# Kernel optimization log

Hardware: AMD Instinct MI355X
Metric: run time of the kernel (lower is better)

## Reference

```python
import jax, jax.numpy as jnp
import numpy as np

N, C, K, G, E = 65536, 256, 128, 32, 2097152
LN_EPS = 1e-5


def setup_inputs() -> dict:
    key = jax.random.key(0)
    ks = jax.random.split(key, 16)
    inp = {
        "x": jax.random.normal(ks[0], (N, C), jnp.float32),
        "evals_batch": jax.random.uniform(ks[1], (G * K,), jnp.float32),
        "evecs": jax.random.normal(ks[2], (N, K), jnp.float32),
        "mass": jax.random.uniform(ks[3], (N,), jnp.float32),
        "row": jax.random.randint(ks[4], (E,), 0, N),
        "col": jax.random.randint(ks[5], (E,), 0, N),
        "vals": jax.random.normal(ks[6], (E,), jnp.float32),
        # learned parameters (torch Linear convention: weight is [out, in])
        "t_params": jnp.full((C,), 0.5, jnp.float32),
        "grad_W": jax.random.normal(ks[7], (C, C), jnp.float32) / np.sqrt(C),
        "grad_b": jnp.zeros((C,), jnp.float32),
        "W1": jax.random.normal(ks[8], (C, 2 * C), jnp.float32) / np.sqrt(2 * C),
        "b1": jnp.zeros((C,), jnp.float32),
        "W2": jax.random.normal(ks[9], (C, C), jnp.float32) / np.sqrt(C),
        "b2": jnp.zeros((C,), jnp.float32),
        "ln_g": jnp.ones((C,), jnp.float32),
        "ln_b": jnp.zeros((C,), jnp.float32),
    }
    return inp


def reference(x, evals_batch, evecs, mass, row, col, vals,
              t_params, grad_W, grad_b, W1, b1, W2, b2, ln_g, ln_b):
    # batch is contiguous with G equal-size graphs of n nodes each
    n = N // G
    t = jnp.abs(t_params)                                   # [C]
    xg = x.reshape(G, n, C)
    eg = evecs.reshape(G, n, K)
    mg = mass.reshape(G, n)
    ev = evals_batch.reshape(G, K)
    # spectral diffusion, batched over graphs
    x_spec = jnp.einsum('gnk,gnc->gkc', eg, xg * mg[..., None])      # [G,K,C]
    decay = jnp.exp(-t[None, None, :] * jnp.clip(ev, 0.0)[..., None])  # [G,K,C]
    diff_out = jnp.einsum('gnk,gkc->gnc', eg, x_spec * decay).reshape(N, C)
    # sparse gradient operator: grad_feat = grad_X_sparse @ x  (COO)
    grad_feat = jax.ops.segment_sum(vals[:, None] * x[col], row, num_segments=N)
    grad_feat = grad_feat @ grad_W.T + grad_b
    # MLP (dropout is identity at eval)
    fused = jnp.concatenate([diff_out, grad_feat], axis=-1)           # [N,2C]
    h = jax.nn.relu(fused @ W1.T + b1)
    fused = h @ W2.T + b2
    # residual + LayerNorm
    y = x + fused
    mu = jnp.mean(y, axis=-1, keepdims=True)
    var = jnp.var(y, axis=-1, keepdims=True)
    return (y - mu) * jax.lax.rsqrt(var + LN_EPS) * ln_g + ln_b
```

## Files before the change

### kernel.cpp

```cpp
#include <hip/hip_runtime.h>

typedef unsigned short u16;
typedef unsigned long long u64;
using short8 = __attribute__((ext_vector_type(8))) short;
using f32x4  = __attribute__((ext_vector_type(4))) float;

constexpr int N_  = 65536;
constexpr int C_  = 256;
constexpr int K_  = 128;
constexpr int G_  = 32;
constexpr int NG_ = 2048;
constexpr int E_  = 2097152;
constexpr int NBIN_ = 2048;
constexpr int CAPB_ = 1280;
constexpr int NCHK_ = 256;

__device__ __forceinline__ u16 f2bf(float f) {
  unsigned u = __float_as_uint(f);
  unsigned r = u + 0x7FFF + ((u >> 16) & 1);
  return (u16)(r >> 16);
}
__device__ __forceinline__ float bf2f(u16 h) { return __uint_as_float((unsigned)h << 16); }

__device__ __forceinline__ void gload_lds16(const void* g, void* l) {
  __builtin_amdgcn_global_load_lds((const __attribute__((address_space(1))) void*)g,
                                   (__attribute__((address_space(3))) void*)l, 16, 0, 0);
}

constexpr int PA_HIST = NCHK_;
constexpr int PA_CVX  = 4096;
constexpr int PA_CVE  = 2048;
constexpr int PA_W1   = 512;
constexpr int PA_W2   = 256;
constexpr int PA_T256 = 16;
constexpr int PA_BC   = 16;
constexpr int PA_TOTAL = PA_HIST + PA_CVX + PA_CVE + PA_W1 + PA_W2 + PA_T256 + PA_BC;

__global__ __launch_bounds__(256) void k_phaseA(
    const int* __restrict__ row, int* __restrict__ bh,
    const float* __restrict__ x, const float* __restrict__ mass,
    u16* __restrict__ xbf, u16* __restrict__ xmT,
    const float* __restrict__ evecs, u16* __restrict__ Ebf, u16* __restrict__ EbfT,
    const float* __restrict__ W1, u16* __restrict__ W1bf,
    const float* __restrict__ W2, u16* __restrict__ W2bf,
    const float* __restrict__ gW, u16* __restrict__ gWT,
    const float* __restrict__ gb, const float* __restrict__ b1, float* __restrict__ bc) {
  __shared__ __align__(16) char smem[64 * 65 * 4 + 256];
  float (*tile)[65] = (float(*)[65])smem;
  float* msm = (float*)(smem + 64 * 65 * 4);
  int id = blockIdx.x, tid = threadIdx.x;

  if (id < PA_HIST) {
    int* hist = (int*)smem;
    #pragma unroll
    for (int j = 0; j < 8; ++j) hist[tid + j * 256] = 0;
    __syncthreads();
    int e0 = id * 8192 + tid;
    #pragma unroll 4
    for (int i = 0; i < 32; ++i)
      atomicAdd(&hist[row[e0 + i * 256] >> 5], 1);
    __syncthreads();
    #pragma unroll
    for (int j = 0; j < 8; ++j) {
      int bin = tid + j * 256;
      bh[(size_t)bin * NCHK_ + id] = hist[bin];
    }
    return;
  }
  id -= PA_HIST;
  if (id < PA_CVX) {
    int r0 = (id >> 2) * 64, c0 = (id & 3) * 64;
    int tr = tid >> 4, tc4 = (tid & 15) * 4;
    #pragma unroll
    for (int p = 0; p < 4; ++p) {
      int r = p * 16 + tr;
      float4 v = *(const float4*)&x[(size_t)(r0 + r) * C_ + c0 + tc4];
      tile[r][tc4 + 0] = v.x; tile[r][tc4 + 1] = v.y; tile[r][tc4 + 2] = v.z; tile[r][tc4 + 3] = v.w;
      ushort4 o = {f2bf(v.x), f2bf(v.y), f2bf(v.z), f2bf(v.w)};
      *(ushort4*)&xbf[(size_t)(r0 + r) * C_ + c0 + tc4] = o;
    }
    if (tid < 64) msm[tid] = mass[r0 + tid];
    __syncthreads();
    int g = r0 >> 11, n0 = r0 & (NG_ - 1);
    #pragma unroll
    for (int p = 0; p < 4; ++p) {
      int cl = p * 16 + tr;
      ushort4 o;
      o.x = f2bf(tile[tc4 + 0][cl] * msm[tc4 + 0]);
      o.y = f2bf(tile[tc4 + 1][cl] * msm[tc4 + 1]);
      o.z = f2bf(tile[tc4 + 2][cl] * msm[tc4 + 2]);
      o.w = f2bf(tile[tc4 + 3][cl] * msm[tc4 + 3]);
      *(ushort4*)&xmT[((size_t)g * C_ + c0 + cl) * NG_ + n0 + tc4] = o;
    }
    return;
  }
  id -= PA_CVX;
  if (id < PA_CVE) {
    int r0 = (id >> 1) * 64, c0 = (id & 1) * 64;
    int tr = tid >> 4, tc4 = (tid & 15) * 4;
    #pragma unroll
    for (int p = 0; p < 4; ++p) {
      int r = p * 16 + tr;
      float4 v = *(const float4*)&evecs[(size_t)(r0 + r) * K_ + c0 + tc4];
      tile[r][tc4 + 0] = v.x; tile[r][tc4 + 1] = v.y; tile[r][tc4 + 2] = v.z; tile[r][tc4 + 3] = v.w;
      ushort4 o = {f2bf(v.x), f2bf(v.y), f2bf(v.z), f2bf(v.w)};
      *(ushort4*)&Ebf[(size_t)(r0 + r) * K_ + c0 + tc4] = o;
    }
    __syncthreads();
    int g = r0 >> 11, n0 = r0 & (NG_ - 1);
    #pragma unroll
    for (int p = 0; p < 4; ++p) {
      int cl = p * 16 + tr;
      ushort4 o = {f2bf(tile[tc4 + 0][cl]), f2bf(tile[tc4 + 1][cl]),
                   f2bf(tile[tc4 + 2][cl]), f2bf(tile[tc4 + 3][cl])};
      *(ushort4*)&EbfT[((size_t)g * K_ + c0 + cl) * NG_ + n0 + tc4] = o;
    }
    return;
  }
  id -= PA_CVE;
  if (id < PA_W1) { int i = id * 256 + tid; W1bf[i] = f2bf(W1[i]); return; }
  id -= PA_W1;
  if (id < PA_W2) { int i = id * 256 + tid; W2bf[i] = f2bf(W2[i]); return; }
  id -= PA_W2;
  if (id < PA_T256) {
    int r0 = (id & 3) * 64, c0 = (id >> 2) * 64;
    int tr = tid >> 4, tc4 = (tid & 15) * 4;
    #pragma unroll
    for (int p = 0; p < 4; ++p) {
      int r = p * 16 + tr;
      float4 v = *(const float4*)&gW[(size_t)(r0 + r) * 256 + c0 + tc4];
      tile[r][tc4 + 0] = v.x; tile[r][tc4 + 1] = v.y; tile[r][tc4 + 2] = v.z; tile[r][tc4 + 3] = v.w;
    }
    __syncthreads();
    #pragma unroll
    for (int p = 0; p < 4; ++p) {
      int cl = p * 16 + tr;
      ushort4 o = {f2bf(tile[tc4 + 0][cl]), f2bf(tile[tc4 + 1][cl]),
                   f2bf(tile[tc4 + 2][cl]), f2bf(tile[tc4 + 3][cl])};
      *(ushort4*)&gWT[(size_t)(c0 + cl) * 256 + r0 + tc4] = o;
    }
    return;
  }
  id -= PA_T256;
  {
    float* red = (float*)smem;
    int cl = tid >> 4, js = tid & 15;
    int c = id * 16 + cl;
    const float* wrow = &W1[(size_t)c * 512 + 256 + js * 16];
    float s = 0.f;
    #pragma unroll
    for (int jj = 0; jj < 16; ++jj) s += wrow[jj] * gb[js * 16 + jj];
    red[cl * 17 + js] = s;
    __syncthreads();
    if (js == 0) {
      float tot = b1[c];
      #pragma unroll
      for (int q = 0; q < 16; ++q) tot += red[cl * 17 + q];
      bc[c] = tot;
    }
  }
}

__global__ __launch_bounds__(256) void k_scanOS(const int* __restrict__ bh, int* __restrict__ baseL,
                                                int* __restrict__ gcnt) {
  __shared__ int sc[256];
  int bin = blockIdx.x, tid = threadIdx.x;
  int v = bh[(size_t)bin * NCHK_ + tid];
  sc[tid] = v;
  __syncthreads();
  for (int o = 1; o < 256; o <<= 1) {
    int t = (tid >= o) ? sc[tid - o] : 0;
    __syncthreads();
    sc[tid] += t;
    __syncthreads();
  }
  baseL[(size_t)tid * NBIN_ + bin] = sc[tid] - v;
  if (tid == 255) gcnt[bin] = sc[255];
}

__global__ __launch_bounds__(256) void k_scatterOS(const int* __restrict__ row, const int* __restrict__ col,
                                                   const float* __restrict__ vals, const int* __restrict__ baseL,
                                                   u64* __restrict__ epB) {
  __shared__ int sbase[NBIN_];
  __shared__ int cur[NBIN_];
  int id = blockIdx.x, tid = threadIdx.x;
  #pragma unroll
  for (int j = 0; j < 8; ++j) {
    int b = tid + j * 256;
    sbase[b] = baseL[(size_t)id * NBIN_ + b];
    cur[b] = 0;
  }
  __syncthreads();
  int e0 = id * 8192 + tid;
  #pragma unroll 4
  for (int i = 0; i < 32; ++i) {
    int e = e0 + i * 256;
    int rr = row[e];
    int b = rr >> 5;
    int rk = atomicAdd(&cur[b], 1);
    int lpos = sbase[b] + rk;
    if (lpos < CAPB_)
      epB[(size_t)b * CAPB_ + lpos] =
          ((u64)(rr & 31) << 32) | ((u64)f2bf(vals[e]) << 16) | (u64)(unsigned)col[e];
  }
}

__global__ __launch_bounds__(256) void k_gatherE(const u16* __restrict__ xbf, const int* __restrict__ gcnt,
                                                 const u64* __restrict__ epB, u16* __restrict__ gf) {
  __shared__ unsigned eL[CAPB_];
  __shared__ int chist[256], ccur[256];
  __shared__ int roff[257];
  __shared__ int sc[256];
  int b = blockIdx.x, tid = threadIdx.x;
  int wave = tid >> 6, lane = tid & 63;
  int n = gcnt[b]; if (n > CAPB_) n = CAPB_;
  chist[tid] = 0; ccur[tid] = 0;
  __syncthreads();
  const u64* ebase = epB + (size_t)b * CAPB_;
  for (int i = tid; i < n; i += 256) {
    u64 pk = ebase[i];
    int cell = (int)((pk & 0xFFFFu) >> 13) * 32 + ((int)(pk >> 32) & 31);
    atomicAdd(&chist[cell], 1);
  }
  __syncthreads();
  int s = chist[tid];
  sc[tid] = s;
  __syncthreads();
  for (int o = 1; o < 256; o <<= 1) {
    int v = (tid >= o) ? sc[tid - o] : 0;
    __syncthreads();
    sc[tid] += v;
    __syncthreads();
  }
  roff[tid] = sc[tid] - s;
  if (tid == 255) roff[256] = sc[255];
  __syncthreads();
  for (int i = tid; i < n; i += 256) {
    u64 pk = ebase[i];
    int cell = (int)((pk & 0xFFFFu) >> 13) * 32 + ((int)(pk >> 32) & 31);
    int rk = atomicAdd(&ccur[cell], 1);
    eL[roff[cell] + rk] = (unsigned)pk;
  }
  __syncthreads();

  const u16* xb = xbf + lane * 4;
  f32x4 acc[8];
  #pragma unroll
  for (int k = 0; k < 8; ++k) acc[k] = {0.f, 0.f, 0.f, 0.f};
  for (int t = 0; t < 8; ++t) {
    #pragma unroll
    for (int k = 0; k < 8; ++k) {
      int cell = t * 32 + wave * 8 + k;
      int j = roff[cell], en = roff[cell + 1];
      while (j < en) {
        unsigned u[4]; ushort4 xv[4];
        #pragma unroll
        for (int q = 0; q < 4; ++q) u[q] = (j + q < en) ? eL[j + q] : 0u;
        #pragma unroll
        for (int q = 0; q < 4; ++q) xv[q] = *(const ushort4*)(xb + (size_t)(u[q] & 0xFFFFu) * C_);
        #pragma unroll
        for (int q = 0; q < 4; ++q) {
          float v = bf2f((u16)(u[q] >> 16));
          acc[k][0] += v * bf2f(xv[q].x); acc[k][1] += v * bf2f(xv[q].y);
          acc[k][2] += v * bf2f(xv[q].z); acc[k][3] += v * bf2f(xv[q].w);
        }
        j += 4;
      }
    }
    __syncthreads();
  }
  int r0 = b * 32 + wave * 8;
  #pragma unroll
  for (int k = 0; k < 8; ++k) {
    ushort4 o = {f2bf(acc[k][0]), f2bf(acc[k][1]), f2bf(acc[k][2]), f2bf(acc[k][3])};
    *(ushort4*)&gf[(size_t)(r0 + k) * C_ + lane * 4] = o;
  }
}

constexpr int EPI_BF16  = 0;
constexpr int EPI_DECAY = 3;
constexpr int EPI_TRANS = 4;

template <int BM, int BN, int EPI>
__global__ __launch_bounds__(256) void k_gemm(
    const u16* __restrict__ A, long sAz, int lda,
    const u16* __restrict__ B, long sBz, int ldb,
    int Kd,
    void* __restrict__ outp, long sCz, int ldc,
    const float* __restrict__ tpar, const float* __restrict__ evptr) {
  constexpr int WM = BM / 2, WN = BN / 2;
  constexpr int FM = WM / 16, FN = WN / 16;
  __shared__ __align__(16) u16 Asm[BM * 32];
  __shared__ __align__(16) u16 Bsm[BN * 32];
  int z = blockIdx.z;
  const u16* Ab = A + (long)z * sAz + (long)blockIdx.x * BM * lda;
  const u16* Bb = B + (long)z * sBz + (long)blockIdx.y * BN * ldb;
  int tid = threadIdx.x;
  int wave = tid >> 6, lane = tid & 63;
  int wm = wave >> 1, wn = wave & 1;

  f32x4 acc[FM][FN];
  #pragma unroll
  for (int m = 0; m < FM; ++m)
    #pragma unroll
    for (int n = 0; n < FN; ++n) acc[m][n] = {0.f, 0.f, 0.f, 0.f};

  const u16* aA = Ab + (size_t)(wave * 16 + (lane >> 2)) * lda + (lane & 3) * 8;
  const u16* aB = Bb + (size_t)(wave * 16 + (lane >> 2)) * ldb + (lane & 3) * 8;
  u16* lA = Asm + wave * 512;
  u16* lB = Bsm + wave * 512;
  int arow = wm * WM + (lane & 15);
  int brow = wn * WN + (lane & 15);
  int kof = (lane >> 4) * 8;

  for (int k0 = 0; k0 < Kd; k0 += 32) {
    #pragma unroll
    for (int j = 0; j < BM / 64; ++j) gload_lds16(aA + (size_t)j * 64 * lda + k0, lA + j * 2048);
    #pragma unroll
    for (int j = 0; j < BN / 64; ++j) gload_lds16(aB + (size_t)j * 64 * ldb + k0, lB + j * 2048);
    __syncthreads();
    short8 af[FM], bfr[FN];
    #pragma unroll
    for (int m = 0; m < FM; ++m) af[m] = *(const short8*)(Asm + (arow + m * 16) * 32 + kof);
    #pragma unroll
    for (int n = 0; n < FN; ++n) bfr[n] = *(const short8*)(Bsm + (brow + n * 16) * 32 + kof);
    #pragma unroll
    for (int m = 0; m < FM; ++m)
      #pragma unroll
      for (int n = 0; n < FN; ++n)
        acc[m][n] = __builtin_amdgcn_mfma_f32_16x16x32_bf16(af[m], bfr[n], acc[m][n], 0, 0, 0);
    __syncthreads();
  }

  #pragma unroll
  for (int m = 0; m < FM; ++m) {
    #pragma unroll
    for (int n = 0; n < FN; ++n) {
      int cc = blockIdx.y * BN + wn * WN + n * 16 + (lane & 15);
      int rb = blockIdx.x * BM + wm * WM + m * 16 + ((lane >> 4) << 2);
      if constexpr (EPI == EPI_TRANS) {
        ushort4 o = {f2bf(acc[m][n][0]), f2bf(acc[m][n][1]), f2bf(acc[m][n][2]), f2bf(acc[m][n][3])};
        *(ushort4*)((u16*)outp + (long)z * sCz + (long)cc * ldc + rb) = o;
      } else if constexpr (EPI == EPI_DECAY) {
        float tv = fabsf(tpar[cc]);
        #pragma unroll
        for (int r = 0; r < 4; ++r) {
          float ee = fmaxf(evptr[(size_t)z * K_ + rb + r], 0.f);
          ((u16*)outp)[(long)z * sCz + (long)(rb + r) * ldc + cc] = f2bf(acc[m][n][r] * __expf(-tv * ee));
        }
      } else {
        #pragma unroll
        for (int r = 0; r < 4; ++r)
          ((u16*)outp)[(long)z * sCz + (long)(rb + r) * ldc + cc] = f2bf(acc[m][n][r]);
      }
    }
  }
}

__global__ __launch_bounds__(256) void k_gemm_h2(
    const u16* __restrict__ Eb, const u16* __restrict__ Tt,
    const u16* __restrict__ gf, const u16* __restrict__ Wc,
    const float* __restrict__ bc, u16* __restrict__ h) {
  __shared__ __align__(16) u16 Asm[128 * 32];
  __shared__ __align__(16) u16 Bsm[128 * 32];
  int i0 = blockIdx.x * 128;
  int g = i0 >> 11;
  int tid = threadIdx.x, wave = tid >> 6, lane = tid & 63;
  int wm = wave >> 1, wn = wave & 1;
  f32x4 acc[4][4];
  #pragma unroll
  for (int m = 0; m < 4; ++m)
    #pragma unroll
    for (int n = 0; n < 4; ++n) acc[m][n] = {0.f, 0.f, 0.f, 0.f};
  int srow = wave * 16 + (lane >> 2), scol = (lane & 3) * 8;
  u16* lA = Asm + wave * 512;
  u16* lB = Bsm + wave * 512;
  int arow = wm * 64 + (lane & 15);
  int brow = wn * 64 + (lane & 15);
  int kof = (lane >> 4) * 8;

  {
    const u16* aA = Eb + (size_t)(i0 + srow) * K_ + scol;
    const u16* aB = Tt + (size_t)g * C_ * K_ + (size_t)(blockIdx.y * 128 + srow) * K_ + scol;
    for (int k0 = 0; k0 < 128; k0 += 32) {
      gload_lds16(aA + k0, lA); gload_lds16(aA + (size_t)64 * K_ + k0, lA + 2048);
      gload_lds16(aB + k0, lB); gload_lds16(aB + (size_t)64 * K_ + k0, lB + 2048);
      __syncthreads();
      short8 af[4], bfr[4];
      #pragma unroll
      for (int m = 0; m < 4; ++m) af[m] = *(const short8*)(Asm + (arow + m * 16) * 32 + kof);
      #pragma unroll
      for (int n = 0; n < 4; ++n) bfr[n] = *(const short8*)(Bsm + (brow + n * 16) * 32 + kof);
      #pragma unroll
      for (int m = 0; m < 4; ++m)
        #pragma unroll
        for (int n = 0; n < 4; ++n)
          acc[m][n] = __builtin_amdgcn_mfma_f32_16x16x32_bf16(af[m], bfr[n], acc[m][n], 0, 0, 0);
      __syncthreads();
    }
  }
  {
    const u16* aA = gf + (size_t)(i0 + srow) * C_ + scol;
    const u16* aB = Wc + (size_t)(blockIdx.y * 128 + srow) * C_ + scol;
    for (int k0 = 0; k0 < 256; k0 += 32) {
      gload_lds16(aA + k0, lA); gload_lds16(aA + (size_t)64 * C_ + k0, lA + 2048);
      gload_lds16(aB + k0, lB); gload_lds16(aB + (size_t)64 * C_ + k0, lB + 2048);
      __syncthreads();
      short8 af[4], bfr[4];
      #pragma unroll
      for (int m = 0; m < 4; ++m) af[m] = *(const short8*)(Asm + (arow + m * 16) * 32 + kof);
      #pragma unroll
      for (int n = 0; n < 4; ++n) bfr[n] = *(const short8*)(Bsm + (brow + n * 16) * 32 + kof);
      #pragma unroll
      for (int m = 0; m < 4; ++m)
        #pragma unroll
        for (int n = 0; n < 4; ++n)
          acc[m][n] = __builtin_amdgcn_mfma_f32_16x16x32_bf16(af[m], bfr[n], acc[m][n], 0, 0, 0);
      __syncthreads();
    }
  }
  #pragma unroll
  for (int m = 0; m < 4; ++m) {
    #pragma unroll
    for (int n = 0; n < 4; ++n) {
      int cc = blockIdx.y * 128 + wn * 64 + n * 16 + (lane & 15);
      int rb = i0 + wm * 64 + m * 16 + ((lane >> 4) << 2);
      float bv = bc[cc];
      #pragma unroll
      for (int r = 0; r < 4; ++r)
        h[(size_t)(rb + r) * C_ + cc] = f2bf(fmaxf(acc[m][n][r] + bv, 0.f));
    }
  }
}

__global__ __launch_bounds__(512) void k_out(
    const u16* __restrict__ h, const u16* __restrict__ W2bf, const float* __restrict__ b2,
    const float* __restrict__ x, const float* __restrict__ lng, const float* __restrict__ lnb,
    float* __restrict__ out) {
  __shared__ __align__(16) u16 Asm[128 * 32];
  __shared__ __align__(16) u16 Bsm[256 * 32];
  __shared__ float ps1[128][4], ps2[128][4];
  int i0 = blockIdx.x * 128;
  int tid = threadIdx.x, wave = tid >> 6, lane = tid & 63;
  int wm = wave >> 2, wn = wave & 3;

  f32x4 acc[4][4];
  #pragma unroll
  for (int m = 0; m < 4; ++m)
    #pragma unroll
    for (int n = 0; n < 4; ++n) acc[m][n] = {0.f, 0.f, 0.f, 0.f};

  const u16* aA = h + (size_t)(i0 + (tid >> 2)) * C_ + (tid & 3) * 8;
  const u16* aB = W2bf + (size_t)(tid >> 2) * C_ + (tid & 3) * 8;
  u16* lA = Asm + wave * 512;
  u16* lB = Bsm + wave * 512;
  int arow = wm * 64 + (lane & 15);
  int brow = wn * 64 + (lane & 15);
  int kof = (lane >> 4) * 8;

  for (int k0 = 0; k0 < 256; k0 += 32) {
    gload_lds16(aA + k0, lA);
    gload_lds16(aB + k0, lB);
    gload_lds16(aB + (size_t)128 * C_ + k0, lB + 4096);
    __syncthreads();
    short8 af[4], bfr[4];
    #pragma unroll
    for (int m = 0; m < 4; ++m) af[m] = *(const short8*)(Asm + (arow + m * 16) * 32 + kof);
    #pragma unroll
    for (int n = 0; n < 4; ++n) bfr[n] = *(const short8*)(Bsm + (brow + n * 16) * 32 + kof);
    #pragma unroll
    for (int m = 0; m < 4; ++m)
      #pragma unroll
      for (int n = 0; n < 4; ++n)
        acc[m][n] = __builtin_amdgcn_mfma_f32_16x16x32_bf16(af[m], bfr[n], acc[m][n], 0, 0, 0);
    __syncthreads();
  }

  float bb[4], lg[4], lb[4];
  #pragma unroll
  for (int n = 0; n < 4; ++n) {
    int cc = wn * 64 + n * 16 + (lane & 15);
    bb[n] = b2[cc]; lg[n] = lng[cc]; lb[n] = lnb[cc];
  }
  #pragma unroll
  for (int m = 0; m < 4; ++m) {
    #pragma unroll
    for (int r = 0; r < 4; ++r) {
      int rl = wm * 64 + m * 16 + ((lane >> 4) << 2) + r;
      #pragma unroll
      for (int n = 0; n < 4; ++n) {
        int cc = wn * 64 + n * 16 + (lane & 15);
        acc[m][n][r] += bb[n] + x[(size_t)(i0 + rl) * C_ + cc];
      }
    }
  }
  #pragma unroll
  for (int m = 0; m < 4; ++m) {
    #pragma unroll
    for (int r = 0; r < 4; ++r) {
      float t1 = acc[m][0][r] + acc[m][1][r] + acc[m][2][r] + acc[m][3][r];
      float t2 = acc[m][0][r] * acc[m][0][r] + acc[m][1][r] * acc[m][1][r] +
                 acc[m][2][r] * acc[m][2][r] + acc[m][3][r] * acc[m][3][r];
      #pragma unroll
      for (int msk = 1; msk < 16; msk <<= 1) {
        t1 += __shfl_xor(t1, msk);
        t2 += __shfl_xor(t2, msk);
      }
      if ((lane & 15) == 0) {
        int rl = wm * 64 + m * 16 + ((lane >> 4) << 2) + r;
        ps1[rl][wn] = t1; ps2[rl][wn] = t2;
      }
    }
  }
  __syncthreads();
  #pragma unroll
  for (int m = 0; m < 4; ++m) {
    #pragma unroll
    for (int r = 0; r < 4; ++r) {
      int rl = wm * 64 + m * 16 + ((lane >> 4) << 2) + r;
      float tot1 = ps1[rl][0] + ps1[rl][1] + ps1[rl][2] + ps1[rl][3];
      float tot2 = ps2[rl][0] + ps2[rl][1] + ps2[rl][2] + ps2[rl][3];
      float mu = tot1 * (1.f / 256.f);
      float var = fmaxf(tot2 * (1.f / 256.f) - mu * mu, 0.f);
      float rs = rsqrtf(var + 1e-5f);
      #pragma unroll
      for (int n = 0; n < 4; ++n) {
        int cc = wn * 64 + n * 16 + (lane & 15);
        out[(size_t)(i0 + rl) * C_ + cc] = (acc[m][n][r] - mu) * rs * lg[n] + lb[n];
      }
    }
  }
}

extern "C" void kernel_launch(void* const* d_in, const int* in_sizes, int n_in,
                              void* d_out, int out_size, void* d_ws, size_t ws_size,
                              hipStream_t stream) {
  const float* x        = (const float*)d_in[0];
  const float* ev       = (const float*)d_in[1];
  const float* evecs    = (const float*)d_in[2];
  const float* mass     = (const float*)d_in[3];
  const int*   row      = (const int*)d_in[4];
  const int*   col      = (const int*)d_in[5];
  const float* vals     = (const float*)d_in[6];
  const float* t_params = (const float*)d_in[7];
  const float* gW       = (const float*)d_in[8];
  const float* gb       = (const float*)d_in[9];
  const float* W1       = (const float*)d_in[10];
  const float* b1       = (const float*)d_in[11];
  const float* W2       = (const float*)d_in[12];
  const float* b2       = (const float*)d_in[13];
  const float* lng      = (const float*)d_in[14];
  const float* lnb      = (const float*)d_in[15];
  float* out = (float*)d_out;

  char* p = (char*)d_ws;
  u16* xbf  = (u16*)p; p += (size_t)N_ * C_ * 2;
  u16* xmT  = (u16*)p; p += (size_t)G_ * C_ * NG_ * 2;
  u16* EbfT = (u16*)p; p += (size_t)G_ * K_ * NG_ * 2;
  u16* Ebf  = (u16*)p; p += (size_t)N_ * K_ * 2;
  u16* S    = (u16*)p; p += (size_t)G_ * K_ * C_ * 2;
  u16* Tt   = (u16*)p; p += (size_t)G_ * C_ * K_ * 2;
  u16* h    = (u16*)p; p += (size_t)N_ * C_ * 2;
  u16* W1bf = (u16*)p; p += (size_t)C_ * 512 * 2;
  u16* W2bf = (u16*)p; p += (size_t)C_ * C_ * 2;
  u16* gWT  = (u16*)p; p += (size_t)C_ * C_ * 2;
  u16* Wc   = (u16*)p; p += (size_t)C_ * C_ * 2;
  float* bc = (float*)p; p += (size_t)C_ * 4;
  int* gcnt = (int*)p; p += (size_t)NBIN_ * 4;
  int* bh   = (int*)p; p += (size_t)NBIN_ * NCHK_ * 4;
  int* baseL= (int*)p; p += (size_t)NCHK_ * NBIN_ * 4;
  u64* epB  = (u64*)p; p += (size_t)NBIN_ * CAPB_ * 8;
  u16* gf   = xmT;

  k_phaseA<<<PA_TOTAL, 256, 0, stream>>>(row, bh, x, mass, xbf, xmT,
                                         evecs, Ebf, EbfT, W1, W1bf, W2, W2bf,
                                         gW, gWT, gb, b1, bc);
  k_scanOS<<<NBIN_, 256, 0, stream>>>(bh, baseL, gcnt);
  k_scatterOS<<<NCHK_, 256, 0, stream>>>(row, col, vals, baseL, epB);

  k_gemm<128, 128, EPI_BF16><<<dim3(2, 2, 1), 256, 0, stream>>>(
      W1bf + 256, 0, 512, gWT, 0, 256, 256, Wc, 0, 256, nullptr, nullptr);
  k_gemm<64, 128, EPI_DECAY><<<dim3(K_ / 64, C_ / 128, G_), 256, 0, stream>>>(
      EbfT, (long)K_ * NG_, NG_, xmT, (long)C_ * NG_, NG_, NG_,
      S, (long)K_ * C_, C_, t_params, ev);
  k_gemm<128, 128, EPI_TRANS><<<dim3(1, 2, G_), 256, 0, stream>>>(
      S, (long)K_ * C_, C_, W1bf, 0, 512, 256,
      Tt, (long)C_ * K_, K_, nullptr, nullptr);

  k_gatherE<<<NBIN_, 256, 0, stream>>>(xbf, gcnt, epB, gf);

  k_gemm_h2<<<dim3(N_ / 128, 2), 256, 0, stream>>>(Ebf, Tt, gf, Wc, bc, h);

  k_out<<<N_ / 128, 512, 0, stream>>>(h, W2bf, b2, x, lng, lnb, out);
}
```

Before: 365.2 us.

## Fuse scatter and small GEMMs into one launch; register-cache edges in gather

Merges the COO scatter kernel, the Wc weight-product GEMM and the spectral decay GEMM into a single heterogeneous launch, with GEMM code moved into a reusable device body. This removes two kernel launches and lets the independent work run concurrently. The gather kernel now keeps each thread's packed edges, cells and ranks in registers from the histogram pass, so edge data is read from global memory once instead of twice. x and the edge values switch from bf16 to fp16 storage for the sparse gather, which changes rounding and risks overflow for large magnitudes.

```diff
diff --git a/kernel.cpp b/kernel.cpp
--- a/kernel.cpp
+++ b/kernel.cpp
@@ -4,6 +4,7 @@
 typedef unsigned long long u64;
 using short8 = __attribute__((ext_vector_type(8))) short;
 using f32x4  = __attribute__((ext_vector_type(4))) float;
+using h16x4  = __attribute__((ext_vector_type(4))) _Float16;
 
 constexpr int N_  = 65536;
 constexpr int C_  = 256;
@@ -21,268 +22,24 @@
   return (u16)(r >> 16);
 }
 __device__ __forceinline__ float bf2f(u16 h) { return __uint_as_float((unsigned)h << 16); }
+__device__ __forceinline__ u16 f2h(float f) {
+  _Float16 h = (_Float16)f;
+  u16 b; __builtin_memcpy(&b, &h, 2);
+  return b;
+}
 
 __device__ __forceinline__ void gload_lds16(const void* g, void* l) {
   __builtin_amdgcn_global_load_lds((const __attribute__((address_space(1))) void*)g,
                                    (__attribute__((address_space(3))) void*)l, 16, 0, 0);
 }
 
-constexpr int PA_HIST = NCHK_;
-constexpr int PA_CVX  = 4096;
-constexpr int PA_CVE  = 2048;
-constexpr int PA_W1   = 512;
-constexpr int PA_W2   = 256;
-constexpr int PA_T256 = 16;
-constexpr int PA_BC   = 16;
-constexpr int PA_TOTAL = PA_HIST + PA_CVX + PA_CVE + PA_W1 + PA_W2 + PA_T256 + PA_BC;
-
-__global__ __launch_bounds__(256) void k_phaseA(
-    const int* __restrict__ row, int* __restrict__ bh,
-    const float* __restrict__ x, const float* __restrict__ mass,
-    u16* __restrict__ xbf, u16* __restrict__ xmT,
-    const float* __restrict__ evecs, u16* __restrict__ Ebf, u16* __restrict__ EbfT,
-    const float* __restrict__ W1, u16* __restrict__ W1bf,
-    const float* __restrict__ W2, u16* __restrict__ W2bf,
-    const float* __restrict__ gW, u16* __restrict__ gWT,
-    const float* __restrict__ gb, const float* __restrict__ b1, float* __restrict__ bc) {
-  __shared__ __align__(16) char smem[64 * 65 * 4 + 256];
-  float (*tile)[65] = (float(*)[65])smem;
-  float* msm = (float*)(smem + 64 * 65 * 4);
-  int id = blockIdx.x, tid = threadIdx.x;
-
-  if (id < PA_HIST) {
-    int* hist = (int*)smem;
-    #pragma unroll
-    for (int j = 0; j < 8; ++j) hist[tid + j * 256] = 0;
-    __syncthreads();
-    int e0 = id * 8192 + tid;
-    #pragma unroll 4
-    for (int i = 0; i < 32; ++i)
-      atomicAdd(&hist[row[e0 + i * 256] >> 5], 1);
-    __syncthreads();
-    #pragma unroll
-    for (int j = 0; j < 8; ++j) {
-      int bin = tid + j * 256;
-      bh[(size_t)bin * NCHK_ + id] = hist[bin];
-    }
-    return;
-  }
-  id -= PA_HIST;
-  if (id < PA_CVX) {
-    int r0 = (id >> 2) * 64, c0 = (id & 3) * 64;
-    int tr = tid >> 4, tc4 = (tid & 15) * 4;
-    #pragma unroll
-    for (int p = 0; p < 4; ++p) {
-      int r = p * 16 + tr;
-      float4 v = *(const float4*)&x[(size_t)(r0 + r) * C_ + c0 + tc4];
-      tile[r][tc4 + 0] = v.x; tile[r][tc4 + 1] = v.y; tile[r][tc4 + 2] = v.z; tile[r][tc4 + 3] = v.w;
-      ushort4 o = {f2bf(v.x), f2bf(v.y), f2bf(v.z), f2bf(v.w)};
-      *(ushort4*)&xbf[(size_t)(r0 + r) * C_ + c0 + tc4] = o;
-    }
-    if (tid < 64) msm[tid] = mass[r0 + tid];
-    __syncthreads();
-    int g = r0 >> 11, n0 = r0 & (NG_ - 1);
-    #pragma unroll
-    for (int p = 0; p < 4; ++p) {
-      int cl = p * 16 + tr;
-      ushort4 o;
-      o.x = f2bf(tile[tc4 + 0][cl] * msm[tc4 + 0]);
-      o.y = f2bf(tile[tc4 + 1][cl] * msm[tc4 + 1]);
-      o.z = f2bf(tile[tc4 + 2][cl] * msm[tc4 + 2]);
-      o.w = f2bf(tile[tc4 + 3][cl] * msm[tc4 + 3]);
-      *(ushort4*)&xmT[((size_t)g * C_ + c0 + cl) * NG_ + n0 + tc4] = o;
-    }
-    return;
-  }
-  id -= PA_CVX;
-  if (id < PA_CVE) {
-    int r0 = (id >> 1) * 64, c0 = (id & 1) * 64;
-    int tr = tid >> 4, tc4 = (tid & 15) * 4;
-    #pragma unroll
-    for (int p = 0; p < 4; ++p) {
-      int r = p * 16 + tr;
-      float4 v = *(const float4*)&evecs[(size_t)(r0 + r) * K_ + c0 + tc4];
-      tile[r][tc4 + 0] = v.x; tile[r][tc4 + 1] = v.y; tile[r][tc4 + 2] = v.z; tile[r][tc4 + 3] = v.w;
-      ushort4 o = {f2bf(v.x), f2bf(v.y), f2bf(v.z), f2bf(v.w)};
-      *(ushort4*)&Ebf[(size_t)(r0 + r) * K_ + c0 + tc4] = o;
-    }
-    __syncthreads();
-    int g = r0 >> 11, n0 = r0 & (NG_ - 1);
-    #pragma unroll
-    for (int p = 0; p < 4; ++p) {
-      int cl = p * 16 + tr;
-      ushort4 o = {f2bf(tile[tc4 + 0][cl]), f2bf(tile[tc4 + 1][cl]),
-                   f2bf(tile[tc4 + 2][cl]), f2bf(tile[tc4 + 3][cl])};
-      *(ushort4*)&EbfT[((size_t)g * K_ + c0 + cl) * NG_ + n0 + tc4] = o;
-    }
-    return;
-  }
-  id -= PA_CVE;
-  if (id < PA_W1) { int i = id * 256 + tid; W1bf[i] = f2bf(W1[i]); return; }
-  id -= PA_W1;
-  if (id < PA_W2) { int i = id * 256 + tid; W2bf[i] = f2bf(W2[i]); return; }
-  id -= PA_W2;
-  if (id < PA_T256) {
-    int r0 = (id & 3) * 64, c0 = (id >> 2) * 64;
-    int tr = tid >> 4, tc4 = (tid & 15) * 4;
-    #pragma unroll
-    for (int p = 0; p < 4; ++p) {
-      int r = p * 16 + tr;
-      float4 v = *(const float4*)&gW[(size_t)(r0 + r) * 256 + c0 + tc4];
-      tile[r][tc4 + 0] = v.x; tile[r][tc4 + 1] = v.y; tile[r][tc4 + 2] = v.z; tile[r][tc4 + 3] = v.w;
-    }
-    __syncthreads();
-    #pragma unroll
-    for (int p = 0; p < 4; ++p) {
-      int cl = p * 16 + tr;
-      ushort4 o = {f2bf(tile[tc4 + 0][cl]), f2bf(tile[tc4 + 1][cl]),
-                   f2bf(tile[tc4 + 2][cl]), f2bf(tile[tc4 + 3][cl])};
-      *(ushort4*)&gWT[(size_t)(c0 + cl) * 256 + r0 + tc4] = o;
-    }
-    return;
-  }
-  id -= PA_T256;
-  {
-    float* red = (float*)smem;
-    int cl = tid >> 4, js = tid & 15;
-    int c = id * 16 + cl;
-    const float* wrow = &W1[(size_t)c * 512 + 256 + js * 16];
-    float s = 0.f;
-    #pragma unroll
-    for (int jj = 0; jj < 16; ++jj) s += wrow[jj] * gb[js * 16 + jj];
-    red[cl * 17 + js] = s;
-    __syncthreads();
-    if (js == 0) {
-      float tot = b1[c];
-      #pragma unroll
-      for (int q = 0; q < 16; ++q) tot += red[cl * 17 + q];
-      bc[c] = tot;
-    }
-  }
-}
-
-__global__ __launch_bounds__(256) void k_scanOS(const int* __restrict__ bh, int* __restrict__ baseL,
-                                                int* __restrict__ gcnt) {
-  __shared__ int sc[256];
-  int bin = blockIdx.x, tid = threadIdx.x;
-  int v = bh[(size_t)bin * NCHK_ + tid];
-  sc[tid] = v;
-  __syncthreads();
-  for (int o = 1; o < 256; o <<= 1) {
-    int t = (tid >= o) ? sc[tid - o] : 0;
-    __syncthreads();
-    sc[tid] += t;
-    __syncthreads();
-  }
-  baseL[(size_t)tid * NBIN_ + bin] = sc[tid] - v;
-  if (tid == 255) gcnt[bin] = sc[255];
-}
-
-__global__ __launch_bounds__(256) void k_scatterOS(const int* __restrict__ row, const int* __restrict__ col,
-                                                   const float* __restrict__ vals, const int* __restrict__ baseL,
-                                                   u64* __restrict__ epB) {
-  __shared__ int sbase[NBIN_];
-  __shared__ int cur[NBIN_];
-  int id = blockIdx.x, tid = threadIdx.x;
-  #pragma unroll
-  for (int j = 0; j < 8; ++j) {
-    int b = tid + j * 256;
-    sbase[b] = baseL[(size_t)id * NBIN_ + b];
-    cur[b] = 0;
-  }
-  __syncthreads();
-  int e0 = id * 8192 + tid;
-  #pragma unroll 4
-  for (int i = 0; i < 32; ++i) {
-    int e = e0 + i * 256;
-    int rr = row[e];
-    int b = rr >> 5;
-    int rk = atomicAdd(&cur[b], 1);
-    int lpos = sbase[b] + rk;
-    if (lpos < CAPB_)
-      epB[(size_t)b * CAPB_ + lpos] =
-          ((u64)(rr & 31) << 32) | ((u64)f2bf(vals[e]) << 16) | (u64)(unsigned)col[e];
-  }
-}
-
-__global__ __launch_bounds__(256) void k_gatherE(const u16* __restrict__ xbf, const int* __restrict__ gcnt,
-                                                 const u64* __restrict__ epB, u16* __restrict__ gf) {
-  __shared__ unsigned eL[CAPB_];
-  __shared__ int chist[256], ccur[256];
-  __shared__ int roff[257];
-  __shared__ int sc[256];
-  int b = blockIdx.x, tid = threadIdx.x;
-  int wave = tid >> 6, lane = tid & 63;
-  int n = gcnt[b]; if (n > CAPB_) n = CAPB_;
-  chist[tid] = 0; ccur[tid] = 0;
-  __syncthreads();
-  const u64* ebase = epB + (size_t)b * CAPB_;
-  for (int i = tid; i < n; i += 256) {
-    u64 pk = ebase[i];
-    int cell = (int)((pk & 0xFFFFu) >> 13) * 32 + ((int)(pk >> 32) & 31);
-    atomicAdd(&chist[cell], 1);
-  }
-  __syncthreads();
-  int s = chist[tid];
-  sc[tid] = s;
-  __syncthreads();
-  for (int o = 1; o < 256; o <<= 1) {
-    int v = (tid >= o) ? sc[tid - o] : 0;
-    __syncthreads();
-    sc[tid] += v;
-    __syncthreads();
-  }
-  roff[tid] = sc[tid] - s;
-  if (tid == 255) roff[256] = sc[255];
-  __syncthreads();
-  for (int i = tid; i < n; i += 256) {
-    u64 pk = ebase[i];
-    int cell = (int)((pk & 0xFFFFu) >> 13) * 32 + ((int)(pk >> 32) & 31);
-    int rk = atomicAdd(&ccur[cell], 1);
-    eL[roff[cell] + rk] = (unsigned)pk;
-  }
-  __syncthreads();
-
-  const u16* xb = xbf + lane * 4;
-  f32x4 acc[8];
-  #pragma unroll
-  for (int k = 0; k < 8; ++k) acc[k] = {0.f, 0.f, 0.f, 0.f};
-  for (int t = 0; t < 8; ++t) {
-    #pragma unroll
-    for (int k = 0; k < 8; ++k) {
-      int cell = t * 32 + wave * 8 + k;
-      int j = roff[cell], en = roff[cell + 1];
-      while (j < en) {
-        unsigned u[4]; ushort4 xv[4];
-        #pragma unroll
-        for (int q = 0; q < 4; ++q) u[q] = (j + q < en) ? eL[j + q] : 0u;
-        #pragma unroll
-        for (int q = 0; q < 4; ++q) xv[q] = *(const ushort4*)(xb + (size_t)(u[q] & 0xFFFFu) * C_);
-        #pragma unroll
-        for (int q = 0; q < 4; ++q) {
-          float v = bf2f((u16)(u[q] >> 16));
-          acc[k][0] += v * bf2f(xv[q].x); acc[k][1] += v * bf2f(xv[q].y);
-          acc[k][2] += v * bf2f(xv[q].z); acc[k][3] += v * bf2f(xv[q].w);
-        }
-        j += 4;
-      }
-    }
-    __syncthreads();
-  }
-  int r0 = b * 32 + wave * 8;
-  #pragma unroll
-  for (int k = 0; k < 8; ++k) {
-    ushort4 o = {f2bf(acc[k][0]), f2bf(acc[k][1]), f2bf(acc[k][2]), f2bf(acc[k][3])};
-    *(ushort4*)&gf[(size_t)(r0 + k) * C_ + lane * 4] = o;
-  }
-}
-
 constexpr int EPI_BF16  = 0;
 constexpr int EPI_DECAY = 3;
 constexpr int EPI_TRANS = 4;
 
 template <int BM, int BN, int EPI>
-__global__ __launch_bounds__(256) void k_gemm(
+__device__ __forceinline__ void gemm_body(
+    char* smem, int bx, int by, int z,
     const u16* __restrict__ A, long sAz, int lda,
     const u16* __restrict__ B, long sBz, int ldb,
     int Kd,
@@ -290,11 +47,10 @@
     const float* __restrict__ tpar, const float* __restrict__ evptr) {
   constexpr int WM = BM / 2, WN = BN / 2;
   constexpr int FM = WM / 16, FN = WN / 16;
-  __shared__ __align__(16) u16 Asm[BM * 32];
-  __shared__ __align__(16) u16 Bsm[BN * 32];
-  int z = blockIdx.z;
-  const u16* Ab = A + (long)z * sAz + (long)blockIdx.x * BM * lda;
-  const u16* Bb = B + (long)z * sBz + (long)blockIdx.y * BN * ldb;
+  u16* Asm = (u16*)smem;
+  u16* Bsm = Asm + BM * 32;
+  const u16* Ab = A + (long)z * sAz + (long)bx * BM * lda;
+  const u16* Bb = B + (long)z * sBz + (long)by * BN * ldb;
   int tid = threadIdx.x;
   int wave = tid >> 6, lane = tid & 63;
   int wm = wave >> 1, wn = wave & 1;
@@ -336,8 +92,8 @@
   for (int m = 0; m < FM; ++m) {
     #pragma unroll
     for (int n = 0; n < FN; ++n) {
-      int cc = blockIdx.y * BN + wn * WN + n * 16 + (lane & 15);
-      int rb = blockIdx.x * BM + wm * WM + m * 16 + ((lane >> 4) << 2);
+      int cc = by * BN + wn * WN + n * 16 + (lane & 15);
+      int rb = bx * BM + wm * WM + m * 16 + ((lane >> 4) << 2);
       if constexpr (EPI == EPI_TRANS) {
         ushort4 o = {f2bf(acc[m][n][0]), f2bf(acc[m][n][1]), f2bf(acc[m][n][2]), f2bf(acc[m][n][3])};
         *(ushort4*)((u16*)outp + (long)z * sCz + (long)cc * ldc + rb) = o;
@@ -354,6 +110,303 @@
           ((u16*)outp)[(long)z * sCz + (long)(rb + r) * ldc + cc] = f2bf(acc[m][n][r]);
       }
     }
+  }
+}
+
+template <int BM, int BN, int EPI>
+__global__ __launch_bounds__(256) void k_gemm(
+    const u16* __restrict__ A, long sAz, int lda,
+    const u16* __restrict__ B, long sBz, int ldb,
+    int Kd,
+    void* __restrict__ outp, long sCz, int ldc,
+    const float* __restrict__ tpar, const float* __restrict__ evptr) {
+  __shared__ __align__(16) char smem[(BM + BN) * 32 * 2];
+  gemm_body<BM, BN, EPI>(smem, blockIdx.x, blockIdx.y, blockIdx.z,
+                         A, sAz, lda, B, sBz, ldb, Kd, outp, sCz, ldc, tpar, evptr);
+}
+
+constexpr int PA_HIST = NCHK_;
+constexpr int PA_CVX  = 4096;
+constexpr int PA_CVE  = 2048;
+constexpr int PA_W1   = 512;
+constexpr int PA_W2   = 256;
+constexpr int PA_T256 = 16;
+constexpr int PA_BC   = 16;
+constexpr int PA_TOTAL = PA_HIST + PA_CVX + PA_CVE + PA_W1 + PA_W2 + PA_T256 + PA_BC;
+
+__global__ __launch_bounds__(256) void k_phaseA(
+    const int* __restrict__ row, int* __restrict__ bh,
+    const float* __restrict__ x, const float* __restrict__ mass,
+    u16* __restrict__ xhf, u16* __restrict__ xmT,
+    const float* __restrict__ evecs, u16* __restrict__ Ebf, u16* __restrict__ EbfT,
+    const float* __restrict__ W1, u16* __restrict__ W1bf,
+    const float* __restrict__ W2, u16* __restrict__ W2bf,
+    const float* __restrict__ gW, u16* __restrict__ gWT,
+    const float* __restrict__ gb, const float* __restrict__ b1, float* __restrict__ bc) {
+  __shared__ __align__(16) char smem[64 * 65 * 4 + 256];
+  float (*tile)[65] = (float(*)[65])smem;
+  float* msm = (float*)(smem + 64 * 65 * 4);
+  int id = blockIdx.x, tid = threadIdx.x;
+
+  if (id < PA_HIST) {
+    int* hist = (int*)smem;
+    #pragma unroll
+    for (int j = 0; j < 8; ++j) hist[tid + j * 256] = 0;
+    __syncthreads();
+    int e0 = id * 8192 + tid;
+    #pragma unroll 4
+    for (int i = 0; i < 32; ++i)
+      atomicAdd(&hist[row[e0 + i * 256] >> 5], 1);
+    __syncthreads();
+    #pragma unroll
+    for (int j = 0; j < 8; ++j) {
+      int bin = tid + j * 256;
+      bh[(size_t)bin * NCHK_ + id] = hist[bin];
+    }
+    return;
+  }
+  id -= PA_HIST;
+  if (id < PA_CVX) {
+    int r0 = (id >> 2) * 64, c0 = (id & 3) * 64;
+    int tr = tid >> 4, tc4 = (tid & 15) * 4;
+    #pragma unroll
+    for (int p = 0; p < 4; ++p) {
+      int r = p * 16 + tr;
+      float4 v = *(const float4*)&x[(size_t)(r0 + r) * C_ + c0 + tc4];
+      tile[r][tc4 + 0] = v.x; tile[r][tc4 + 1] = v.y; tile[r][tc4 + 2] = v.z; tile[r][tc4 + 3] = v.w;
+      ushort4 o = {f2h(v.x), f2h(v.y), f2h(v.z), f2h(v.w)};
+      *(ushort4*)&xhf[(size_t)(r0 + r) * C_ + c0 + tc4] = o;
+    }
+    if (tid < 64) msm[tid] = mass[r0 + tid];
+    __syncthreads();
+    int g = r0 >> 11, n0 = r0 & (NG_ - 1);
+    #pragma unroll
+    for (int p = 0; p < 4; ++p) {
+      int cl = p * 16 + tr;
+      ushort4 o;
+      o.x = f2bf(tile[tc4 + 0][cl] * msm[tc4 + 0]);
+      o.y = f2bf(tile[tc4 + 1][cl] * msm[tc4 + 1]);
+      o.z = f2bf(tile[tc4 + 2][cl] * msm[tc4 + 2]);
+      o.w = f2bf(tile[tc4 + 3][cl] * msm[tc4 + 3]);
+      *(ushort4*)&xmT[((size_t)g * C_ + c0 + cl) * NG_ + n0 + tc4] = o;
+    }
+    return;
+  }
+  id -= PA_CVX;
+  if (id < PA_CVE) {
+    int r0 = (id >> 1) * 64, c0 = (id & 1) * 64;
+    int tr = tid >> 4, tc4 = (tid & 15) * 4;
+    #pragma unroll
+    for (int p = 0; p < 4; ++p) {
+      int r = p * 16 + tr;
+      float4 v = *(const float4*)&evecs[(size_t)(r0 + r) * K_ + c0 + tc4];
+      tile[r][tc4 + 0] = v.x; tile[r][tc4 + 1] = v.y; tile[r][tc4 + 2] = v.z; tile[r][tc4 + 3] = v.w;
+      ushort4 o = {f2bf(v.x), f2bf(v.y), f2bf(v.z), f2bf(v.w)};
+      *(ushort4*)&Ebf[(size_t)(r0 + r) * K_ + c0 + tc4] = o;
+    }
+    __syncthreads();
+    int g = r0 >> 11, n0 = r0 & (NG_ - 1);
+    #pragma unroll
+    for (int p = 0; p < 4; ++p) {
+      int cl = p * 16 + tr;
+      ushort4 o = {f2bf(tile[tc4 + 0][cl]), f2bf(tile[tc4 + 1][cl]),
+                   f2bf(tile[tc4 + 2][cl]), f2bf(tile[tc4 + 3][cl])};
+      *(ushort4*)&EbfT[((size_t)g * K_ + c0 + cl) * NG_ + n0 + tc4] = o;
+    }
+    return;
+  }
+  id -= PA_CVE;
+  if (id < PA_W1) { int i = id * 256 + tid; W1bf[i] = f2bf(W1[i]); return; }
+  id -= PA_W1;
+  if (id < PA_W2) { int i = id * 256 + tid; W2bf[i] = f2bf(W2[i]); return; }
+  id -= PA_W2;
+  if (id < PA_T256) {
+    int r0 = (id & 3) * 64, c0 = (id >> 2) * 64;
+    int tr = tid >> 4, tc4 = (tid & 15) * 4;
+    #pragma unroll
+    for (int p = 0; p < 4; ++p) {
+      int r = p * 16 + tr;
+      float4 v = *(const float4*)&gW[(size_t)(r0 + r) * 256 + c0 + tc4];
+      tile[r][tc4 + 0] = v.x; tile[r][tc4 + 1] = v.y; tile[r][tc4 + 2] = v.z; tile[r][tc4 + 3] = v.w;
+    }
+    __syncthreads();
+    #pragma unroll
+    for (int p = 0; p < 4; ++p) {
+      int cl = p * 16 + tr;
+      ushort4 o = {f2bf(tile[tc4 + 0][cl]), f2bf(tile[tc4 + 1][cl]),
+                   f2bf(tile[tc4 + 2][cl]), f2bf(tile[tc4 + 3][cl])};
+      *(ushort4*)&gWT[(size_t)(c0 + cl) * 256 + r0 + tc4] = o;
+    }
+    return;
+  }
+  id -= PA_T256;
+  {
+    float* red = (float*)smem;
+    int cl = tid >> 4, js = tid & 15;
+    int c = id * 16 + cl;
+    const float* wrow = &W1[(size_t)c * 512 + 256 + js * 16];
+    float s = 0.f;
+    #pragma unroll
+    for (int jj = 0; jj < 16; ++jj) s += wrow[jj] * gb[js * 16 + jj];
+    red[cl * 17 + js] = s;
+    __syncthreads();
+    if (js == 0) {
+      float tot = b1[c];
+      #pragma unroll
+      for (int q = 0; q < 16; ++q) tot += red[cl * 17 + q];
+      bc[c] = tot;
+    }
+  }
+}
+
+__global__ __launch_bounds__(256) void k_scanOS(const int* __restrict__ bh, int* __restrict__ baseL,
+                                                int* __restrict__ gcnt) {
+  __shared__ int sc[256];
+  int bin = blockIdx.x, tid = threadIdx.x;
+  int v = bh[(size_t)bin * NCHK_ + tid];
+  sc[tid] = v;
+  __syncthreads();
+  for (int o = 1; o < 256; o <<= 1) {
+    int t = (tid >= o) ? sc[tid - o] : 0;
+    __syncthreads();
+    sc[tid] += t;
+    __syncthreads();
+  }
+  baseL[(size_t)tid * NBIN_ + bin] = sc[tid] - v;
+  if (tid == 255) gcnt[bin] = sc[255];
+}
+
+constexpr int PB_SCAT = NCHK_;
+constexpr int PB_WC   = 4;
+constexpr int PB_SP1  = 128;
+constexpr int PB_TOTAL = PB_SCAT + PB_WC + PB_SP1;
+
+__global__ __launch_bounds__(256) void k_phaseB(
+    const int* __restrict__ row, const int* __restrict__ col, const float* __restrict__ vals,
+    const int* __restrict__ baseL, u64* __restrict__ epB,
+    const u16* __restrict__ W1bf, const u16* __restrict__ gWT, u16* __restrict__ Wc,
+    const u16* __restrict__ EbfT, const u16* __restrict__ xmT, u16* __restrict__ S,
+    const float* __restrict__ tpar, const float* __restrict__ evptr) {
+  __shared__ __align__(16) char smem[16384];
+  int id = blockIdx.x, tid = threadIdx.x;
+
+  if (id < PB_SCAT) {
+    int* sbase = (int*)smem;
+    int* cur   = sbase + NBIN_;
+    #pragma unroll
+    for (int j = 0; j < 8; ++j) {
+      int b = tid + j * 256;
+      sbase[b] = baseL[(size_t)id * NBIN_ + b];
+      cur[b] = 0;
+    }
+    __syncthreads();
+    int e0 = id * 8192 + tid;
+    #pragma unroll 4
+    for (int i = 0; i < 32; ++i) {
+      int e = e0 + i * 256;
+      int rr = row[e];
+      int b = rr >> 5;
+      int rk = atomicAdd(&cur[b], 1);
+      int lpos = sbase[b] + rk;
+      if (lpos < CAPB_)
+        epB[(size_t)b * CAPB_ + lpos] =
+            ((u64)(rr & 31) << 32) | ((u64)f2h(vals[e]) << 16) | (u64)(unsigned)col[e];
+    }
+    return;
+  }
+  id -= PB_SCAT;
+  if (id < PB_WC) {
+    gemm_body<128, 128, EPI_BF16>(smem, id & 1, id >> 1, 0,
+                                  W1bf + 256, 0, 512, gWT, 0, 256, 256,
+                                  Wc, 0, 256, nullptr, nullptr);
+    return;
+  }
+  id -= PB_WC;
+  {
+    int zz = id >> 2, rem = id & 3;
+    gemm_body<64, 128, EPI_DECAY>(smem, rem & 1, rem >> 1, zz,
+                                  EbfT, (long)K_ * NG_, NG_, xmT, (long)C_ * NG_, NG_, NG_,
+                                  S, (long)K_ * C_, C_, tpar, evptr);
+  }
+}
+
+__global__ __launch_bounds__(256) void k_gatherF(const u16* __restrict__ xhf, const int* __restrict__ gcnt,
+                                                 const u64* __restrict__ epB, u16* __restrict__ gf) {
+  __shared__ unsigned eL[CAPB_];
+  __shared__ int chist[256];
+  __shared__ int roff[257];
+  __shared__ int sc[256];
+  int b = blockIdx.x, tid = threadIdx.x;
+  int wave = tid >> 6, lane = tid & 63;
+  int n = gcnt[b]; if (n > CAPB_) n = CAPB_;
+  chist[tid] = 0;
+  __syncthreads();
+  const u64* ebase = epB + (size_t)b * CAPB_;
+  unsigned pkr[5]; int cellr[5]; int rkr[5];
+  #pragma unroll
+  for (int q = 0; q < 5; ++q) {
+    int i = tid + q * 256;
+    bool ok = i < n;
+    u64 pk = ok ? ebase[i] : 0;
+    int cell = (int)((pk & 0xFFFFu) >> 13) * 32 + ((int)(pk >> 32) & 31);
+    pkr[q] = (unsigned)pk; cellr[q] = cell; rkr[q] = 0;
+    if (ok) rkr[q] = atomicAdd(&chist[cell], 1);
+  }
+  __syncthreads();
+  int s = chist[tid];
+  sc[tid] = s;
+  __syncthreads();
+  for (int o = 1; o < 256; o <<= 1) {
+    int v = (tid >= o) ? sc[tid - o] : 0;
+    __syncthreads();
+    sc[tid] += v;
+    __syncthreads();
+  }
+  roff[tid] = sc[tid] - s;
+  if (tid == 255) roff[256] = sc[255];
+  __syncthreads();
+  #pragma unroll
+  for (int q = 0; q < 5; ++q) {
+    int i = tid + q * 256;
+    if (i < n) eL[roff[cellr[q]] + rkr[q]] = pkr[q];
+  }
+  __syncthreads();
+
+  const u16* xb = xhf + lane * 4;
+  f32x4 acc[8];
+  #pragma unroll
+  for (int k = 0; k < 8; ++k) acc[k] = {0.f, 0.f, 0.f, 0.f};
+  for (int t = 0; t < 8; ++t) {
+    #pragma unroll
+    for (int k = 0; k < 8; ++k) {
+      int cell = t * 32 + wave * 8 + k;
+      int j = roff[cell], en = roff[cell + 1];
+      while (j < en) {
+        unsigned u[4]; h16x4 xv[4];
+        #pragma unroll
+        for (int q = 0; q < 4; ++q) u[q] = (j + q < en) ? eL[j + q] : 0u;
+        #pragma unroll
+        for (int q = 0; q < 4; ++q) xv[q] = *(const h16x4*)(xb + (size_t)(u[q] & 0xFFFFu) * C_);
+        #pragma unroll
+        for (int q = 0; q < 4; ++q) {
+          u16 hb = (u16)(u[q] >> 16);
+          _Float16 hv; __builtin_memcpy(&hv, &hb, 2);
+          float v = (float)hv;
+          acc[k][0] += (float)xv[q][0] * v;
+          acc[k][1] += (float)xv[q][1] * v;
+          acc[k][2] += (float)xv[q][2] * v;
+          acc[k][3] += (float)xv[q][3] * v;
+        }
+        j += 4;
+      }
+    }
+    __syncthreads();
+  }
+  int r0 = b * 32 + wave * 8;
+  #pragma unroll
+  for (int k = 0; k < 8; ++k) {
+    ushort4 o = {f2bf(acc[k][0]), f2bf(acc[k][1]), f2bf(acc[k][2]), f2bf(acc[k][3])};
+    *(ushort4*)&gf[(size_t)(r0 + k) * C_ + lane * 4] = o;
   }
 }
 
@@ -554,7 +607,7 @@
   float* out = (float*)d_out;
 
   char* p = (char*)d_ws;
-  u16* xbf  = (u16*)p; p += (size_t)N_ * C_ * 2;
+  u16* xhf  = (u16*)p; p += (size_t)N_ * C_ * 2;
   u16* xmT  = (u16*)p; p += (size_t)G_ * C_ * NG_ * 2;
   u16* EbfT = (u16*)p; p += (size_t)G_ * K_ * NG_ * 2;
   u16* Ebf  = (u16*)p; p += (size_t)N_ * K_ * 2;
@@ -572,22 +625,17 @@
   u64* epB  = (u64*)p; p += (size_t)NBIN_ * CAPB_ * 8;
   u16* gf   = xmT;
 
-  k_phaseA<<<PA_TOTAL, 256, 0, stream>>>(row, bh, x, mass, xbf, xmT,
+  k_phaseA<<<PA_TOTAL, 256, 0, stream>>>(row, bh, x, mass, xhf, xmT,
                                          evecs, Ebf, EbfT, W1, W1bf, W2, W2bf,
                                          gW, gWT, gb, b1, bc);
   k_scanOS<<<NBIN_, 256, 0, stream>>>(bh, baseL, gcnt);
-  k_scatterOS<<<NCHK_, 256, 0, stream>>>(row, col, vals, baseL, epB);
-
-  k_gemm<128, 128, EPI_BF16><<<dim3(2, 2, 1), 256, 0, stream>>>(
-      W1bf + 256, 0, 512, gWT, 0, 256, 256, Wc, 0, 256, nullptr, nullptr);
-  k_gemm<64, 128, EPI_DECAY><<<dim3(K_ / 64, C_ / 128, G_), 256, 0, stream>>>(
-      EbfT, (long)K_ * NG_, NG_, xmT, (long)C_ * NG_, NG_, NG_,
-      S, (long)K_ * C_, C_, t_params, ev);
+  k_phaseB<<<PB_TOTAL, 256, 0, stream>>>(row, col, vals, baseL, epB,
+                                         W1bf, gWT, Wc, EbfT, xmT, S, t_params, ev);
   k_gemm<128, 128, EPI_TRANS><<<dim3(1, 2, G_), 256, 0, stream>>>(
       S, (long)K_ * C_, C_, W1bf, 0, 512, 256,
       Tt, (long)C_ * K_, K_, nullptr, nullptr);
 
-  k_gatherE<<<NBIN_, 256, 0, stream>>>(xbf, gcnt, epB, gf);
+  k_gatherF<<<NBIN_, 256, 0, stream>>>(xhf, gcnt, epB, gf);
 
   k_gemm_h2<<<dim3(N_ / 128, 2), 256, 0, stream>>>(Ebf, Tt, gf, Wc, bc, h);
 
```

Result: faster. 343.4 us (-6.0%).
